# Kernel tuning notes

Measured on AMD Instinct MI355X. Metric: run time of the kernel, lower is better.

## Reference

```python
import jax, jax.numpy as jnp
import numpy as np

KERNEL = 3
LEAKY_SLOPE = 0.2


def fac(feat, filters, k=KERNEL):
    """Per-pixel dynamic filtering (FAC): unfold feat into kxk taps, weight by
    per-pixel predicted filters, reduce over taps. feat: [N,C,H,W],
    filters: [N, C*k*k, H, W] -> out: [N,C,H,W]."""
    N, C, H, W = feat.shape
    pad = (k - 1) // 2
    fp = jnp.pad(feat, ((0, 0), (0, 0), (pad, pad), (pad, pad)))
    # taps ordered (kh, kw) row-major, matching torch unfold(2,k).unfold(3,k).reshape
    patches = jnp.stack(
        [fp[:, :, i:i + H, j:j + W] for i in range(k) for j in range(k)],
        axis=-1,
    )  # [N,C,H,W,k*k]
    # filters: [N, C*k*k, H, W] -> [N,H,W,C,k*k]  (channel-major over C, tap minor)
    w = filters.transpose(0, 2, 3, 1).reshape(N, H, W, C, k * k)
    out = (patches.transpose(0, 2, 3, 1, 4) * w).sum(-1)  # [N,H,W,C]
    return out.transpose(0, 3, 1, 2)  # [N,C,H,W]


def setup_inputs() -> dict:
    key = jax.random.key(0)
    k1, k2 = jax.random.split(key)
    N, C, H, W = 8, 64, 128, 128
    feature = jax.random.normal(k1, (N, C, H, W), dtype=jnp.float32)
    filters = jax.random.normal(k2, (N, C * KERNEL * KERNEL, H, W), dtype=jnp.float32)
    return {"feature": feature, "filters": filters}


def reference(feature, filters):
    x = fac(feature, filters, KERNEL)
    return jnp.where(x >= 0, x, LEAKY_SLOPE * x)
```

## Files before the change

### kernel.cpp

```cpp
#include <hip/hip_runtime.h>


#define N_ 8
#define C_ 64
#define H_ 128
#define W_ 128

typedef __attribute__((ext_vector_type(4))) float float4v;

__global__ __launch_bounds__(256) void fac_kernel(
    const float* __restrict__ feat,
    const float* __restrict__ filt,
    float* __restrict__ out)
{
    int idx = blockIdx.x * 256 + threadIdx.x;
    int w0   = (idx & 31) << 2;
    int rest = idx >> 5;
    int h    = rest & (H_ - 1);
    rest   >>= 7;
    int c    = rest & (C_ - 1);
    int n    = rest >> 6;

    const float* fbase = feat + ((n * C_ + c) * H_) * W_;
    const float* wbase = filt + (((n * C_ + c) * 9) * H_ + h) * W_ + w0;

    float acc[4] = {0.f, 0.f, 0.f, 0.f};

    #pragma unroll
    for (int kh = 0; kh < 3; ++kh) {
        const int hh = h + kh - 1;
        float r[6];
        if (hh >= 0 && hh < H_) {
            const float* row = fbase + hh * W_;
            const float4v v = *reinterpret_cast<const float4v*>(row + w0);
            r[1] = v[0]; r[2] = v[1]; r[3] = v[2]; r[4] = v[3];
            r[0] = (w0 > 0)      ? row[w0 - 1] : 0.f;
            r[5] = (w0 + 4 < W_) ? row[w0 + 4] : 0.f;
        } else {
            #pragma unroll
            for (int i = 0; i < 6; ++i) r[i] = 0.f;
        }

        #pragma unroll
        for (int kw = 0; kw < 3; ++kw) {
            const float4v wv =
                *reinterpret_cast<const float4v*>(wbase + (kh * 3 + kw) * (H_ * W_));
            #pragma unroll
            for (int j = 0; j < 4; ++j)
                acc[j] += r[j + kw] * wv[j];
        }
    }

    float4v o;
    #pragma unroll
    for (int j = 0; j < 4; ++j)
        o[j] = (acc[j] >= 0.f) ? acc[j] : 0.2f * acc[j];
    *reinterpret_cast<float4v*>(out + ((n * C_ + c) * H_ + h) * W_ + w0) = o;
}

extern "C" void kernel_launch(void* const* d_in, const int* in_sizes, int n_in,
                              void* d_out, int out_size, void* d_ws, size_t ws_size,
                              hipStream_t stream) {
    const float* feat = (const float*)d_in[0];
    const float* filt = (const float*)d_in[1];
    float* out = (float*)d_out;
    const int total_threads = N_ * C_ * H_ * (W_ / 4);
    fac_kernel<<<total_threads / 256, 256, 0, stream>>>(feat, filt, out);
}
```

Measured before the change: 412.6 us.

## Process eight pixels per thread with nontemporal filter loads and output stores

Each thread now computes eight output pixels instead of four, halving the thread count and the halo loads per output. All filter taps for a row are loaded up front with nontemporal loads, and outputs are written with nontemporal stores so streaming data bypasses cache retention. Out-of-range rows are handled branch-free by loading a valid row and multiplying by a 0/1 mask. This trades fewer threads and more registers for less redundant feature traffic and more loads in flight.

After: 414.7 us. No clear change (+0.5%).

```diff
diff --git a/kernel.cpp b/kernel.cpp
--- a/kernel.cpp
+++ b/kernel.cpp
@@ -14,8 +14,8 @@
     float* __restrict__ out)
 {
     int idx = blockIdx.x * 256 + threadIdx.x;
-    int w0   = (idx & 31) << 2;
-    int rest = idx >> 5;
+    int w0   = (idx & 15) << 3;
+    int rest = idx >> 4;
     int h    = rest & (H_ - 1);
     rest   >>= 7;
     int c    = rest & (C_ - 1);
@@ -24,38 +24,54 @@
     const float* fbase = feat + ((n * C_ + c) * H_) * W_;
     const float* wbase = filt + (((n * C_ + c) * 9) * H_ + h) * W_ + w0;
 
-    float acc[4] = {0.f, 0.f, 0.f, 0.f};
+    float acc[8];
+    #pragma unroll
+    for (int i = 0; i < 8; ++i) acc[i] = 0.f;
 
     #pragma unroll
     for (int kh = 0; kh < 3; ++kh) {
         const int hh = h + kh - 1;
-        float r[6];
-        if (hh >= 0 && hh < H_) {
-            const float* row = fbase + hh * W_;
-            const float4v v = *reinterpret_cast<const float4v*>(row + w0);
-            r[1] = v[0]; r[2] = v[1]; r[3] = v[2]; r[4] = v[3];
-            r[0] = (w0 > 0)      ? row[w0 - 1] : 0.f;
-            r[5] = (w0 + 4 < W_) ? row[w0 + 4] : 0.f;
-        } else {
-            #pragma unroll
-            for (int i = 0; i < 6; ++i) r[i] = 0.f;
-        }
+        const bool valid = (hh >= 0) && (hh < H_);
+        const float* row = fbase + (valid ? hh : h) * W_;
+
+        const float4v fv0 = *reinterpret_cast<const float4v*>(row + w0);
+        const float4v fv1 = *reinterpret_cast<const float4v*>(row + w0 + 4);
+        const float  hl0 = (w0 > 0)       ? row[w0 - 1] : 0.f;
+        const float  hl1 = (w0 + 8 < W_)  ? row[w0 + 8] : 0.f;
+
+        const float* tb0 = wbase + (kh * 3 + 0) * (H_ * W_);
+        const float* tb1 = wbase + (kh * 3 + 1) * (H_ * W_);
+        const float* tb2 = wbase + (kh * 3 + 2) * (H_ * W_);
+        const float4v wv00 = __builtin_nontemporal_load(reinterpret_cast<const float4v*>(tb0));
+        const float4v wv01 = __builtin_nontemporal_load(reinterpret_cast<const float4v*>(tb0) + 1);
+        const float4v wv10 = __builtin_nontemporal_load(reinterpret_cast<const float4v*>(tb1));
+        const float4v wv11 = __builtin_nontemporal_load(reinterpret_cast<const float4v*>(tb1) + 1);
+        const float4v wv20 = __builtin_nontemporal_load(reinterpret_cast<const float4v*>(tb2));
+        const float4v wv21 = __builtin_nontemporal_load(reinterpret_cast<const float4v*>(tb2) + 1);
+
+        float r[10];
+        const float vm = valid ? 1.f : 0.f;
+        r[0] = hl0 * vm;
+        #pragma unroll
+        for (int i = 0; i < 4; ++i) { r[1 + i] = fv0[i] * vm; r[5 + i] = fv1[i] * vm; }
+        r[9] = hl1 * vm;
 
         #pragma unroll
-        for (int kw = 0; kw < 3; ++kw) {
-            const float4v wv =
-                *reinterpret_cast<const float4v*>(wbase + (kh * 3 + kw) * (H_ * W_));
-            #pragma unroll
-            for (int j = 0; j < 4; ++j)
-                acc[j] += r[j + kw] * wv[j];
+        for (int j = 0; j < 4; ++j) {
+            acc[j]     += r[j]     * wv00[j] + r[j + 1] * wv10[j] + r[j + 2] * wv20[j];
+            acc[4 + j] += r[4 + j] * wv01[j] + r[5 + j] * wv11[j] + r[6 + j] * wv21[j];
         }
     }
 
-    float4v o;
+    float4v o0, o1;
     #pragma unroll
-    for (int j = 0; j < 4; ++j)
-        o[j] = (acc[j] >= 0.f) ? acc[j] : 0.2f * acc[j];
-    *reinterpret_cast<float4v*>(out + ((n * C_ + c) * H_ + h) * W_ + w0) = o;
+    for (int j = 0; j < 4; ++j) {
+        float a0 = acc[j];     o0[j] = (a0 >= 0.f) ? a0 : 0.2f * a0;
+        float a1 = acc[4 + j]; o1[j] = (a1 >= 0.f) ? a1 : 0.2f * a1;
+    }
+    float* optr = out + ((n * C_ + c) * H_ + h) * W_ + w0;
+    __builtin_nontemporal_store(o0, reinterpret_cast<float4v*>(optr));
+    __builtin_nontemporal_store(o1, reinterpret_cast<float4v*>(optr) + 1);
 }
 
 extern "C" void kernel_launch(void* const* d_in, const int* in_sizes, int n_in,
@@ -64,6 +80,6 @@
     const float* feat = (const float*)d_in[0];
     const float* filt = (const float*)d_in[1];
     float* out = (float*)d_out;
-    const int total_threads = N_ * C_ * H_ * (W_ / 4);
+    const int total_threads = N_ * C_ * H_ * (W_ / 8);
     fac_kernel<<<total_threads / 256, 256, 0, stream>>>(feat, filt, out);
 }
```
